# Optimization experiments

Measured on AMD Instinct MI355X. Metric: run time of the kernel, lower is better.

Reference implementation:

```python
import jax, jax.numpy as jnp
import numpy as np

DIM = 1024; DEPTH = 4; HEADS = 16; DIM_HEAD = 64
INNER = HEADS * DIM_HEAD            # 1024
N_LAT = 64; N_MP = 4; MAX_SEQ = 512
FF_MULT = 4; HID = DIM * FF_MULT    # 4096
B = 32; SEQ = 512
EPS = 1e-5


def _custom_ln(x, g):
    # LayerNorm with gain only (module's custom LayerNorm), biased variance
    mean = x.mean(-1, keepdims=True)
    var = x.var(-1, keepdims=True)
    return (x - mean) * jax.lax.rsqrt(var + EPS) * g


def _std_ln(x, w, b):
    # torch nn.LayerNorm with weight and bias
    mean = x.mean(-1, keepdims=True)
    var = x.var(-1, keepdims=True)
    return (x - mean) * jax.lax.rsqrt(var + EPS) * w + b


def setup_inputs() -> dict:
    key = jax.random.key(0)
    ks = jax.random.split(key, 12)
    w = lambda k, shape: jax.random.normal(k, shape, jnp.float32) * 0.02
    return {
        "x": jax.random.normal(ks[0], (B, SEQ, DIM), jnp.float32),
        "mask": jnp.ones((B, SEQ), dtype=bool),
        "pos_emb": w(ks[1], (MAX_SEQ, DIM)),
        "latents": jax.random.normal(ks[2], (N_LAT, DIM), jnp.float32),
        "mp_ln_g": jnp.ones((DIM,), jnp.float32),
        "mp_w": w(ks[3], (DIM, DIM * N_MP)),
        "mp_b": jnp.zeros((DIM * N_MP,), jnp.float32),
        "attn_norm_w": jnp.ones((DEPTH, DIM), jnp.float32),
        "attn_norm_b": jnp.zeros((DEPTH, DIM), jnp.float32),
        "attn_lat_w": jnp.ones((DEPTH, DIM), jnp.float32),
        "attn_lat_b": jnp.zeros((DEPTH, DIM), jnp.float32),
        "Wq": w(ks[4], (DEPTH, DIM, INNER)),
        "Wkv": w(ks[5], (DEPTH, DIM, 2 * INNER)),
        "Wout": w(ks[6], (DEPTH, INNER, DIM)),
        "out_ln_w": jnp.ones((DEPTH, DIM), jnp.float32),
        "out_ln_b": jnp.zeros((DEPTH, DIM), jnp.float32),
        "ff_ln1_g": jnp.ones((DEPTH, DIM), jnp.float32),
        "ff_w1": w(ks[7], (DEPTH, DIM, HID)),
        "ff_ln2_g": jnp.ones((DEPTH, HID), jnp.float32),
        "ff_w2": w(ks[8], (DEPTH, HID, DIM)),
    }


def _forward(x, mask, pos_emb, latents, mp_ln_g, mp_w, mp_b,
             attn_norm_w, attn_norm_b, attn_lat_w, attn_lat_b,
             Wq, Wkv, Wout, out_ln_w, out_ln_b,
             ff_ln1_g, ff_w1, ff_ln2_g, ff_w2):
    b, n, d = x.shape
    x_pos = x + pos_emb[:n]                              # [b, n, d]
    lat = jnp.broadcast_to(latents, (b,) + latents.shape)  # [b, 64, d]

    # latents from mean-pooled sequence (mask in torch code is all-ones)
    pooled = x.mean(axis=1)                              # [b, d]
    mp_lat = (_custom_ln(pooled, mp_ln_g) @ mp_w + mp_b).reshape(b, N_MP, d)
    lat = jnp.concatenate([mp_lat, lat], axis=1)         # [b, 68, d]
    n_lat = lat.shape[1]

    scale = DIM_HEAD ** -0.5
    pad_mask = jnp.pad(mask, ((0, 0), (0, n_lat)), constant_values=True)  # [b, n+68]
    neg = -jnp.finfo(jnp.float32).max

    def split_heads(t):
        return t.reshape(b, -1, HEADS, DIM_HEAD).transpose(0, 2, 1, 3)  # b h n d

    for i in range(DEPTH):
        # --- PerceiverAttention ---
        xn = _std_ln(x_pos, attn_norm_w[i], attn_norm_b[i])
        ln_ = _std_ln(lat, attn_lat_w[i], attn_lat_b[i])
        q = split_heads(ln_ @ Wq[i]) * scale
        kv = jnp.concatenate([xn, ln_], axis=1) @ Wkv[i]   # [b, n+68, 2*inner]
        k, v = jnp.split(kv, 2, axis=-1)
        k = split_heads(k); v = split_heads(v)
        sim = jnp.einsum('bhid,bhjd->bhij', q, k)          # [b, h, 68, n+68]
        sim = jnp.where(pad_mask[:, None, None, :], sim, neg)
        attn = jax.nn.softmax(sim.astype(jnp.float32), axis=-1).astype(sim.dtype)
        out = jnp.einsum('bhij,bhjd->bhid', attn, v)
        out = out.transpose(0, 2, 1, 3).reshape(b, n_lat, INNER)
        lat = _std_ln(out @ Wout[i], out_ln_w[i], out_ln_b[i]) + lat
        # --- FeedForward ---
        h = _custom_ln(lat, ff_ln1_g[i]) @ ff_w1[i]
        h = jax.nn.gelu(h, approximate=False)              # torch nn.GELU default
        h = _custom_ln(h, ff_ln2_g[i]) @ ff_w2[i]
        lat = h + lat
    return lat


def reference(x, mask, pos_emb, latents, mp_ln_g, mp_w, mp_b,
              attn_norm_w, attn_norm_b, attn_lat_w, attn_lat_b,
              Wq, Wkv, Wout, out_ln_w, out_ln_b,
              ff_ln1_g, ff_w1, ff_ln2_g, ff_w2):
    return _forward(x, mask, pos_emb, latents, mp_ln_g, mp_w, mp_b,
                    attn_norm_w, attn_norm_b, attn_lat_w, attn_lat_b,
                    Wq, Wkv, Wout, out_ln_w, out_ln_b,
                    ff_ln1_g, ff_w1, ff_ln2_g, ff_w2)
```

## Files before the change

kernel.cpp:

```cpp
#include <hip/hip_runtime.h>


typedef __attribute__((ext_vector_type(4))) float f32x4;
typedef __attribute__((ext_vector_type(8))) __bf16 bf16x8;
typedef __attribute__((ext_vector_type(4))) __bf16 bf16x4;

#define BATCH 32
#define SEQL  512
#define DIM   1024
#define HEADS 16
#define DH    64
#define LTOT  68
#define KEYS  580
#define KPAD  640
#define HID   4096
#define LN_EPS 1e-5f
#define MLAT  2176

__device__ __forceinline__ float bf2f(__bf16 v) { return (float)v; }
__device__ __forceinline__ __bf16 f2bf(float v) { return (__bf16)v; }
__device__ __forceinline__ float gelu_f(float v) {
    return 0.5f * v * (1.0f + erff(v * 0.70710678118654752f));
}

__device__ __forceinline__ void gld_lds16(const __bf16* g, __bf16* l) {
    __builtin_amdgcn_global_load_lds(
        (const __attribute__((address_space(1))) void*)g,
        (__attribute__((address_space(3))) void*)l, 16, 0, 0);
}

#define SBAR()   asm volatile("s_barrier" ::: "memory")
#define VMCNT4() asm volatile("s_waitcnt vmcnt(4)" ::: "memory")

__device__ __forceinline__ void block_reduce2(float& a, float& b, float* red) {
#pragma unroll
    for (int m = 32; m > 0; m >>= 1) {
        a += __shfl_xor(a, m, 64);
        b += __shfl_xor(b, m, 64);
    }
    int wid = threadIdx.x >> 6, lane = threadIdx.x & 63;
    __syncthreads();
    if (lane == 0) { red[wid] = a; red[4 + wid] = b; }
    __syncthreads();
    a = red[0] + red[1] + red[2] + red[3];
    b = red[4] + red[5] + red[6] + red[7];
}

__global__ __launch_bounds__(256) void add_pos(const float* __restrict__ x,
                                               const float* __restrict__ pos,
                                               __bf16* __restrict__ xp) {
    const int total4 = (BATCH * SEQL * DIM) / 4;
    const int pos4m = (SEQL * DIM) / 4 - 1;
    for (int i = blockIdx.x * 256 + threadIdx.x; i < total4; i += gridDim.x * 256) {
        f32x4 xv = ((const f32x4*)x)[i];
        f32x4 pv = ((const f32x4*)pos)[i & pos4m];
        bf16x4 o;
#pragma unroll
        for (int j = 0; j < 4; ++j) o[j] = f2bf(xv[j] + pv[j]);
        ((bf16x4*)xp)[i] = o;
    }
}

__global__ __launch_bounds__(256) void pool_mean(const float* __restrict__ x,
                                                 float* __restrict__ pooled) {
    int b = blockIdx.x >> 2;
    int d = ((blockIdx.x & 3) << 8) + threadIdx.x;
    const float* p = x + (size_t)b * SEQL * DIM + d;
    float s = 0.f;
    for (int ss = 0; ss < SEQL; ++ss) s += p[(size_t)ss * DIM];
    pooled[b * DIM + d] = s * (1.f / SEQL);
}

__global__ __launch_bounds__(256) void lat_fill(const float* __restrict__ latents,
                                                float* __restrict__ lat) {
    int i = blockIdx.x * 256 + threadIdx.x;
    int b = i >> 14;
    int rem = i & 16383;
    int r = rem >> 8, d4 = rem & 255;
    ((f32x4*)lat)[(size_t)(b * LTOT + 4 + r) * 256 + d4] = ((const f32x4*)latents)[rem];
}

template <typename Tin, bool STD, int COLS>
__global__ __launch_bounds__(256) void ln_rows(const Tin* __restrict__ in,
                                               __bf16* __restrict__ out,
                                               const float* __restrict__ w,
                                               const float* __restrict__ bb) {
    __shared__ float red[8];
    constexpr int NPT = COLS / 256;
    size_t base = (size_t)blockIdx.x * COLS;
    int t = threadIdx.x;
    int c0 = t * NPT;
    float xv[NPT];
    float s = 0.f, s2 = 0.f;
#pragma unroll
    for (int k4 = 0; k4 < NPT / 4; ++k4) {
        if constexpr (sizeof(Tin) == 2) {
            bf16x4 v = *(const bf16x4*)(in + base + c0 + k4 * 4);
#pragma unroll
            for (int e = 0; e < 4; ++e) {
                float f = bf2f(v[e]);
                xv[k4 * 4 + e] = f; s += f; s2 += f * f;
            }
        } else {
            f32x4 v = *(const f32x4*)((const float*)in + base + c0 + k4 * 4);
#pragma unroll
            for (int e = 0; e < 4; ++e) {
                float f = v[e];
                xv[k4 * 4 + e] = f; s += f; s2 += f * f;
            }
        }
    }
    block_reduce2(s, s2, red);
    float mean = s * (1.f / COLS);
    float var = s2 * (1.f / COLS) - mean * mean;
    float rstd = rsqrtf(var + LN_EPS);
#pragma unroll
    for (int k4 = 0; k4 < NPT / 4; ++k4) {
        f32x4 wv = *(const f32x4*)(w + c0 + k4 * 4);
        f32x4 bv;
        if (STD) bv = *(const f32x4*)(bb + c0 + k4 * 4);
        bf16x4 o;
#pragma unroll
        for (int e = 0; e < 4; ++e) {
            float y = (xv[k4 * 4 + e] - mean) * rstd * wv[e];
            if (STD) y += bv[e];
            o[e] = f2bf(y);
        }
        *(bf16x4*)(out + base + c0 + k4 * 4) = o;
    }
}

__global__ __launch_bounds__(256) void ln_gelu2(const __bf16* __restrict__ pk,
                                                __bf16* __restrict__ out,
                                                const float* __restrict__ g) {
    __shared__ float red[8];
    constexpr int NPT = HID / 256;
    const size_t S = (size_t)MLAT * HID;
    size_t base = (size_t)blockIdx.x * HID;
    int t = threadIdx.x;
    int c0 = t * NPT;
    float xv[NPT];
    float s = 0.f, s2 = 0.f;
#pragma unroll
    for (int k4 = 0; k4 < NPT / 4; ++k4) {
        bf16x4 va = *(const bf16x4*)(pk + base + c0 + k4 * 4);
        bf16x4 vb = *(const bf16x4*)(pk + S + base + c0 + k4 * 4);
#pragma unroll
        for (int e = 0; e < 4; ++e) {
            float f = gelu_f(bf2f(va[e]) + bf2f(vb[e]));
            xv[k4 * 4 + e] = f; s += f; s2 += f * f;
        }
    }
    block_reduce2(s, s2, red);
    float mean = s * (1.f / HID);
    float var = s2 * (1.f / HID) - mean * mean;
    float rstd = rsqrtf(var + LN_EPS);
#pragma unroll
    for (int k4 = 0; k4 < NPT / 4; ++k4) {
        f32x4 gv = *(const f32x4*)(g + c0 + k4 * 4);
        bf16x4 o;
#pragma unroll
        for (int e = 0; e < 4; ++e)
            o[e] = f2bf((xv[k4 * 4 + e] - mean) * rstd * gv[e]);
        *(bf16x4*)(out + base + c0 + k4 * 4) = o;
    }
}

__global__ __launch_bounds__(256) void wout_ln_res(const __bf16* __restrict__ gin,
                                                   float* __restrict__ lat,
                                                   __bf16* __restrict__ ffin,
                                                   const float* __restrict__ w,
                                                   const float* __restrict__ b,
                                                   const float* __restrict__ g1) {
    __shared__ float red[8];
    const size_t SL = (size_t)MLAT * DIM;
    size_t base = (size_t)blockIdx.x * DIM;
    int t = threadIdx.x;
    float xv[4];
    float s = 0.f, s2 = 0.f;
#pragma unroll
    for (int k = 0; k < 4; ++k) {
        size_t idx = base + t + (k << 8);
        float v = bf2f(gin[idx]) + bf2f(gin[idx + SL]) +
                  bf2f(gin[idx + 2 * SL]) + bf2f(gin[idx + 3 * SL]);
        xv[k] = v; s += v; s2 += v * v;
    }
    block_reduce2(s, s2, red);
    float mean = s * (1.f / DIM);
    float var = s2 * (1.f / DIM) - mean * mean;
    float rstd = rsqrtf(var + LN_EPS);
    float yv[4];
    s = 0.f; s2 = 0.f;
#pragma unroll
    for (int k = 0; k < 4; ++k) {
        int c = t + (k << 8);
        float y = (xv[k] - mean) * rstd * w[c] + b[c] + lat[base + c];
        yv[k] = y; s += y; s2 += y * y;
        lat[base + c] = y;
    }
    block_reduce2(s, s2, red);
    float mean2 = s * (1.f / DIM);
    float var2 = s2 * (1.f / DIM) - mean2 * mean2;
    float rstd2 = rsqrtf(var2 + LN_EPS);
#pragma unroll
    for (int k = 0; k < 4; ++k) {
        int c = t + (k << 8);
        ffin[base + c] = f2bf((yv[k] - mean2) * rstd2 * g1[c]);
    }
}

__global__ __launch_bounds__(256) void qkv_red(const __bf16* __restrict__ pk,
                                               __bf16* __restrict__ qb,
                                               __bf16* __restrict__ kvb) {
    const size_t S = (size_t)MLAT * 3072;
    int row = blockIdx.y;
    int n = (blockIdx.x * 256 + threadIdx.x) * 4;
    size_t idx = (size_t)row * 3072 + n;
    bf16x4 a = *(const bf16x4*)(pk + idx);
    bf16x4 b = *(const bf16x4*)(pk + S + idx);
    bf16x4 o;
    if (n < 1024) {
#pragma unroll
        for (int e = 0; e < 4; ++e) o[e] = f2bf((bf2f(a[e]) + bf2f(b[e])) * 0.125f);
        *(bf16x4*)(qb + (size_t)row * 1024 + n) = o;
    } else {
#pragma unroll
        for (int e = 0; e < 4; ++e) o[e] = f2bf(bf2f(a[e]) + bf2f(b[e]));
        int bb = ((row >> 2) * 61681) >> 20;
        int r = row - bb * 68;
        *(bf16x4*)(kvb + (size_t)bb * KEYS * 2048 + (size_t)(512 + r) * 2048 +
                   (n - 1024)) = o;
    }
}

__global__ __launch_bounds__(256) void splitk_add8(const __bf16* __restrict__ p,
                                                   float* __restrict__ lat) {
    const size_t S = (size_t)MLAT * 1024;
    int i = blockIdx.x * 256 + threadIdx.x;
    size_t e0 = (size_t)i * 4;
    f32x4 acc = ((f32x4*)lat)[i];
#pragma unroll
    for (int s = 0; s < 8; ++s) {
        bf16x4 v = *(const bf16x4*)(p + s * S + e0);
#pragma unroll
        for (int e = 0; e < 4; ++e) acc[e] += bf2f(v[e]);
    }
    ((f32x4*)lat)[i] = acc;
}

__global__ __launch_bounds__(256) void transpose_all(
    const float* __restrict__ Wq, const float* __restrict__ Wkv,
    const float* __restrict__ Wout, const float* __restrict__ f1,
    const float* __restrict__ f2,
    __bf16* __restrict__ wqT, __bf16* __restrict__ wkvT,
    __bf16* __restrict__ woutT, __bf16* __restrict__ f1T,
    __bf16* __restrict__ f2T) {
    __shared__ float tile[32][33];
    int bid = blockIdx.x;
    const float* in; __bf16* out; int N, nxs, ti;
    if (bid < 1024)      { in = Wq;  out = wqT;  N = 1024; nxs = 5; ti = bid; }
    else if (bid < 3072) { in = Wkv; out = wkvT; N = 2048; nxs = 6; ti = bid - 1024; }
    else if (bid < 4096) { in = Wout;out = woutT;N = 1024; nxs = 5; ti = bid - 3072; }
    else if (bid < 8192) { in = f1;  out = f1T;  N = 4096; nxs = 7; ti = bid - 4096; }
    else                 { in = f2;  out = f2T;  N = 1024; nxs = 5; ti = bid - 8192; }
    int K = (bid >= 8192) ? 4096 : 1024;
    int n0 = (ti & ((1 << nxs) - 1)) << 5;
    int k0 = (ti >> nxs) << 5;
    int tx = threadIdx.x & 31, ty = threadIdx.x >> 5;
#pragma unroll
    for (int p = 0; p < 4; ++p) {
        int kk = ty + p * 8;
        tile[kk][tx] = in[(size_t)(k0 + kk) * N + n0 + tx];
    }
    __syncthreads();
#pragma unroll
    for (int p = 0; p < 4; ++p) {
        int nn = ty + p * 8;
        out[(size_t)(n0 + nn) * K + k0 + tx] = f2bf(tile[tx][nn]);
    }
}

__global__ __launch_bounds__(256) void transpose_cast(const float* __restrict__ in,
                                                      __bf16* __restrict__ out,
                                                      int K, int N) {
    __shared__ float tile[32][33];
    int n0 = blockIdx.x * 32, k0 = blockIdx.y * 32;
    int tx = threadIdx.x & 31, ty = threadIdx.x >> 5;
#pragma unroll
    for (int p = 0; p < 4; ++p) {
        int kk = ty + p * 8;
        tile[kk][tx] = in[(size_t)(k0 + kk) * N + n0 + tx];
    }
    __syncthreads();
#pragma unroll
    for (int p = 0; p < 4; ++p) {
        int nn = ty + p * 8;
        out[(size_t)(n0 + nn) * K + k0 + tx] = f2bf(tile[tx][nn]);
    }
}

template <int EPI, bool POW2>
__global__ __launch_bounds__(256) void gemm_bf16(
    const __bf16* __restrict__ A, const __bf16* __restrict__ Bt,
    void* __restrict__ C0, void* __restrict__ C1, const float* __restrict__ bias,
    int M, int N, int K, int lda, int ldb, int brs, long long bstride, int ldc,
    float scale, int az, long long cz, int zhalf) {
    __shared__ __bf16 As[128][64];
    __shared__ __bf16 Bs[128][64];
    const int t = threadIdx.x;
    const int m0 = blockIdx.y * 128, n0 = blockIdx.x * 128;
    const int z = blockIdx.z;
    A += (size_t)z * az;
    Bt += (size_t)z * az;
    void* Cout = (z < zhalf) ? C0 : C1;
    const long long zoff = (long long)(z < zhalf ? z : z - zhalf) * cz;
    const int wid = t >> 6, lane = t & 63;
    const int wr = wid >> 1, wc = wid & 1;
    const int lrow = lane & 15;
    const int lr = lane >> 3, lc = lane & 7;
    const int src_col = (lc ^ lr) << 3;
    f32x4 acc[4][4] = {};

    int garow[4], gbrow[4];
#pragma unroll
    for (int it = 0; it < 4; ++it) {
        int r = wid * 8 + it * 32 + lr;
        int gm = m0 + r; garow[it] = gm < M ? gm : M - 1;
        int gn = n0 + r; gbrow[it] = gn < N ? gn : N - 1;
    }

    for (int kt = 0; kt < K; kt += 64) {
#pragma unroll
        for (int it = 0; it < 4; ++it) {
            int rb = wid * 8 + it * 32;
            gld_lds16(A + (size_t)garow[it] * lda + kt + src_col, &As[rb][0]);
            gld_lds16(Bt + (size_t)gbrow[it] * ldb + kt + src_col, &Bs[rb][0]);
        }
        __syncthreads();
#pragma unroll
        for (int kc = 0; kc < 2; ++kc) {
            const int ck = (kc << 2) + (lane >> 4);
            bf16x8 af[4], bfr[4];
#pragma unroll
            for (int f = 0; f < 4; ++f) {
                int ra = wr * 64 + f * 16 + lrow;
                af[f] = *(const bf16x8*)(&As[ra][(ck ^ (ra & 7)) << 3]);
                int rb = wc * 64 + f * 16 + lrow;
                bfr[f] = *(const bf16x8*)(&Bs[rb][(ck ^ (rb & 7)) << 3]);
            }
#pragma unroll
            for (int fm = 0; fm < 4; ++fm)
#pragma unroll
                for (int fn = 0; fn < 4; ++fn)
                    acc[fm][fn] = __builtin_amdgcn_mfma_f32_16x16x32_bf16(
                        af[fm], bfr[fn], acc[fm][fn], 0, 0, 0);
        }
        __syncthreads();
    }
    const int rbase = (lane >> 4) << 2;
    const int cofs = lane & 15;
    const int msk = POW2 ? (int)((1u << brs) - 1u) : 0;
#pragma unroll
    for (int fm = 0; fm < 4; ++fm) {
#pragma unroll
        for (int j = 0; j < 4; ++j) {
            int m = m0 + wr * 64 + fm * 16 + rbase + j;
            if (m >= M) continue;
            long long roff;
            if (POW2) roff = (long long)(m >> brs) * bstride + (long long)(m & msk) * ldc;
            else      roff = (long long)(m / brs) * bstride + (long long)(m % brs) * ldc;
            roff += zoff;
#pragma unroll
            for (int fn = 0; fn < 4; ++fn) {
                int n = n0 + wc * 64 + fn * 16 + cofs;
                if (n >= N) continue;
                float v = acc[fm][fn][j];
                if (bias) v += bias[n];
                if (EPI == 0) ((float*)Cout)[roff + n] = v;
                else if (EPI == 1) ((__bf16*)Cout)[roff + n] = f2bf(v);
                else if (EPI == 2) ((__bf16*)Cout)[roff + n] = f2bf(v * scale);
                else ((float*)Cout)[roff + n] = gelu_f(v);
            }
        }
    }
}

template <int EPI>
__global__ __launch_bounds__(512, 2) void gemm256(
    const __bf16* __restrict__ A, const __bf16* __restrict__ Bt,
    void* __restrict__ Cout, const float* __restrict__ bias,
    int M, int N, int K, int brs, long long bstride, int ldc, float scale,
    int gxs) {
    __shared__ __bf16 As[2][256][64];
    __shared__ __bf16 Bs[2][256][64];
    const int t = threadIdx.x;
    const int wid = t >> 6, lane = t & 63;
    const int wr = wid >> 2, wc = wid & 3;
    const int lrow = lane & 15, lk = lane >> 4;
    const int lr8 = lane >> 3;
    const int scol = ((lane & 7) ^ lr8) << 3;

    int nwg = gridDim.x;
    int L = blockIdx.x;
    if ((nwg & 7) == 0) L = (L & 7) * (nwg >> 3) + (L >> 3);
    const int bx = L & ((1 << gxs) - 1), by = L >> gxs;
    const int m0 = by * 256, n0 = bx * 256;

    unsigned aoff[4], boff[4];
#pragma unroll
    for (int h = 0; h < 2; ++h)
#pragma unroll
        for (int rnd = 0; rnd < 2; ++rnd) {
            int r = h * 128 + rnd * 64 + wid * 8 + lr8;
            int gm = m0 + r; if (gm > M - 1) gm = M - 1;
            aoff[h * 2 + rnd] = (unsigned)(gm * K + scol);
            int gn = n0 + r; if (gn > N - 1) gn = N - 1;
            boff[h * 2 + rnd] = (unsigned)(gn * K + scol);
        }

    auto stgA = [&](int buf, int tile, int h) {
        int kt = tile << 6;
        gld_lds16(A + aoff[h * 2 + 0] + kt, &As[buf][h * 128 + wid * 8][0]);
        gld_lds16(A + aoff[h * 2 + 1] + kt, &As[buf][h * 128 + 64 + wid * 8][0]);
    };
    auto stgB = [&](int buf, int tile, int h) {
        int kt = tile << 6;
        gld_lds16(Bt + boff[h * 2 + 0] + kt, &Bs[buf][h * 128 + wid * 8][0]);
        gld_lds16(Bt + boff[h * 2 + 1] + kt, &Bs[buf][h * 128 + 64 + wid * 8][0]);
    };

    f32x4 acc[8][4] = {};
    bf16x8 AF0[4][2], AF1[4][2], BF[2][2], BF2[2][2];

    auto rdAF = [&](bf16x8 (&AF)[4][2], int buf, int qm) {
#pragma unroll
        for (int i = 0; i < 4; ++i) {
            int ra = wr * 128 + (qm * 4 + i) * 16 + lrow;
            AF[i][0] = *(const bf16x8*)(&As[buf][ra][((lk) ^ (ra & 7)) << 3]);
            AF[i][1] = *(const bf16x8*)(&As[buf][ra][((4 + lk) ^ (ra & 7)) << 3]);
        }
    };
    auto rdBF = [&](bf16x8 (&BV)[2][2], int buf, int qn) {
#pragma unroll
        for (int i = 0; i < 2; ++i) {
            int rb = wc * 64 + (qn * 2 + i) * 16 + lrow;
            BV[i][0] = *(const bf16x8*)(&Bs[buf][rb][((lk) ^ (rb & 7)) << 3]);
            BV[i][1] = *(const bf16x8*)(&Bs[buf][rb][((4 + lk) ^ (rb & 7)) << 3]);
        }
    };
    auto mfq = [&](bf16x8 (&AF)[4][2], bf16x8 (&BV)[2][2], int mo, int no) {
        __builtin_amdgcn_s_setprio(1);
#pragma unroll
        for (int i = 0; i < 4; ++i)
#pragma unroll
            for (int nf = 0; nf < 2; ++nf)
#pragma unroll
                for (int ks = 0; ks < 2; ++ks)
                    acc[mo + i][no + nf] = __builtin_amdgcn_mfma_f32_16x16x32_bf16(
                        AF[i][ks], BV[nf][ks], acc[mo + i][no + nf], 0, 0, 0);
        __builtin_amdgcn_s_setprio(0);
    };

    const int nt = K >> 6;
    stgA(0, 0, 0); stgA(0, 0, 1);
    stgB(0, 0, 0); stgB(0, 0, 1);
    stgA(1, 1, 0); stgA(1, 1, 1);
    VMCNT4();
    SBAR();

    for (int tt = 0; tt < nt; tt += 2) {
        const int t1 = tt + 1;
        const int t2 = (tt + 2 < nt) ? tt + 2 : nt - 1;
        const int t3 = (tt + 3 < nt) ? tt + 3 : nt - 1;
        rdAF(AF0, 0, 0); rdBF(BF, 0, 0);
        stgB(1, t1, 0);
        SBAR();
        mfq(AF0, BF, 0, 0);
        SBAR();
        rdAF(AF1, 0, 1);
        stgB(1, t1, 1);
        SBAR();
        mfq(AF1, BF, 4, 0);
        SBAR();
        rdBF(BF2, 0, 1);
        stgA(0, t2, 0);
        SBAR();
        mfq(AF1, BF2, 4, 2);
        SBAR();
        stgA(0, t2, 1);
        SBAR();
        mfq(AF0, BF2, 0, 2);
        VMCNT4();
        SBAR();
        rdAF(AF0, 1, 0); rdBF(BF, 1, 0);
        stgB(0, t2, 0);
        SBAR();
        mfq(AF0, BF, 0, 0);
        SBAR();
        rdAF(AF1, 1, 1);
        stgB(0, t2, 1);
        SBAR();
        mfq(AF1, BF, 4, 0);
        SBAR();
        rdBF(BF2, 1, 1);
        stgA(1, t3, 0);
        SBAR();
        mfq(AF1, BF2, 4, 2);
        SBAR();
        stgA(1, t3, 1);
        SBAR();
        mfq(AF0, BF2, 0, 2);
        VMCNT4();
        SBAR();
    }

    const int rbase = (lane >> 4) << 2;
    const int cofs = lane & 15;
    const int msk = (int)((1u << brs) - 1u);
#pragma unroll
    for (int mf = 0; mf < 8; ++mf) {
#pragma unroll
        for (int j = 0; j < 4; ++j) {
            int m = m0 + wr * 128 + mf * 16 + rbase + j;
            if (m >= M) continue;
            long long roff = (long long)(m >> brs) * bstride +
                             (long long)(m & msk) * ldc;
#pragma unroll
            for (int nf = 0; nf < 4; ++nf) {
                int n = n0 + wc * 64 + nf * 16 + cofs;
                if (n >= N) continue;
                float v = acc[mf][nf][j];
                if (bias) v += bias[n];
                if (EPI == 1) ((__bf16*)Cout)[roff + n] = f2bf(v);
                else if (EPI == 3) ((float*)Cout)[roff + n] = gelu_f(v);
                else ((float*)Cout)[roff + n] = v;
            }
        }
    }
}

__global__ __launch_bounds__(256) void vt_tr(const __bf16* __restrict__ kv,
                                             __bf16* __restrict__ vt) {
    __shared__ __bf16 tile[32][34];
    const int bh = blockIdx.x, b = bh >> 4, h = bh & 15;
    const int k0 = blockIdx.y * 32, d0 = blockIdx.z * 32;
    const int tx = threadIdx.x & 31, ty = threadIdx.x >> 5;
    const __bf16* vbase = kv + (size_t)b * KEYS * 2048 + 1024 + h * DH;
#pragma unroll
    for (int p = 0; p < 4; ++p) {
        int kk = k0 + ty + p * 8;
        int kc = kk < KEYS ? kk : KEYS - 1;
        tile[ty + p * 8][tx] = vbase[(size_t)kc * 2048 + d0 + tx];
    }
    __syncthreads();
    __bf16* obase = vt + (size_t)bh * DH * KPAD;
#pragma unroll
    for (int p = 0; p < 4; ++p) {
        int nn = ty + p * 8;
        __bf16 val = (k0 + tx < KEYS) ? tile[tx][nn] : (__bf16)0.f;
        obase[(size_t)(d0 + nn) * KPAD + k0 + tx] = val;
    }
}

__global__ __launch_bounds__(256) void fused_attn(const __bf16* __restrict__ q,
                                                  const __bf16* __restrict__ kv,
                                                  const __bf16* __restrict__ vt,
                                                  __bf16* __restrict__ ao) {
    __shared__ __bf16 Qs[80][64];
    __shared__ __bf16 Ks[2][64][64];
    __shared__ __bf16 Ps[80][640];
    __shared__ float rowpm[4][80];
    __shared__ float rowm[80];
    __shared__ float rowl[80];

    const int bh = blockIdx.x, b = bh >> 4, h = bh & 15;
    const int t = threadIdx.x, w = t >> 6, lane = t & 63;
    const int lrow = lane & 15;
    const int rbase = (lane >> 4) << 2, cofs = lane & 15;
    const int lr = lane >> 3, lc = lane & 7;
    const int src_col = (lc ^ lr) << 3;

    const __bf16* qbase = q + (size_t)b * LTOT * DIM + h * DH;
    const bf16x8 zero8 = {};
    for (int s = t; s < 80 * 8; s += 256) {
        int r = s >> 3, c8 = s & 7;
        bf16x8 v = zero8;
        if (r < LTOT) v = *(const bf16x8*)(qbase + (size_t)r * DIM + (c8 << 3));
        *(bf16x8*)(&Qs[r][(c8 ^ (r & 7)) << 3]) = v;
    }

    const __bf16* kbase = kv + (size_t)b * KEYS * 2048 + h * DH;
    const __bf16* vbase = vt + (size_t)bh * DH * KPAD;

    auto stageK = [&](int buf, int kt) {
#pragma unroll
        for (int rnd = 0; rnd < 2; ++rnd) {
            int r8 = w * 16 + rnd * 8;
            int gk = kt * 64 + r8 + lr; if (gk > KEYS - 1) gk = KEYS - 1;
            gld_lds16(kbase + (size_t)gk * 2048 + src_col, &Ks[buf][r8][0]);
        }
    };
    auto stageV = [&](int buf, int kt) {
#pragma unroll
        for (int rnd = 0; rnd < 2; ++rnd) {
            int r8 = w * 16 + rnd * 8;
            gld_lds16(vbase + (size_t)(r8 + lr) * KPAD + kt * 64 + src_col,
                      &Ks[buf][r8][0]);
        }
    };

    float pmax[5][4];
#pragma unroll
    for (int fm = 0; fm < 5; ++fm)
#pragma unroll
        for (int j = 0; j < 4; ++j) pmax[fm][j] = -3.0e38f;

    stageK(0, 0);
    __syncthreads();
    for (int kt = 0; kt < 10; ++kt) {
        if (kt < 9) stageK((kt + 1) & 1, kt + 1);
        f32x4 acc[5] = {};
#pragma unroll
        for (int kc = 0; kc < 2; ++kc) {
            int ck = (kc << 2) + (lane >> 4);
            int rb = w * 16 + lrow;
            bf16x8 bfr = *(const bf16x8*)(&Ks[kt & 1][rb][(ck ^ (rb & 7)) << 3]);
#pragma unroll
            for (int fm = 0; fm < 5; ++fm) {
                int ra = fm * 16 + lrow;
                bf16x8 af = *(const bf16x8*)(&Qs[ra][(ck ^ (ra & 7)) << 3]);
                acc[fm] = __builtin_amdgcn_mfma_f32_16x16x32_bf16(
                    af, bfr, acc[fm], 0, 0, 0);
            }
        }
        int key = kt * 64 + w * 16 + cofs;
        int c8 = key >> 3, e = key & 7;
#pragma unroll
        for (int fm = 0; fm < 5; ++fm) {
#pragma unroll
            for (int j = 0; j < 4; ++j) {
                int qrow = fm * 16 + rbase + j;
                float v = (key < KEYS) ? acc[fm][j] : -1.0e30f;
                pmax[fm][j] = fmaxf(pmax[fm][j], v);
                int swz = ((c8 & 7) ^ (qrow & 7)) | (c8 & ~7);
                Ps[qrow][swz * 8 + e] = f2bf(v);
            }
        }
        __syncthreads();
    }
#pragma unroll
    for (int fm = 0; fm < 5; ++fm)
#pragma unroll
        for (int j = 0; j < 4; ++j) {
            float m = pmax[fm][j];
            m = fmaxf(m, __shfl_xor(m, 1, 64));
            m = fmaxf(m, __shfl_xor(m, 2, 64));
            m = fmaxf(m, __shfl_xor(m, 4, 64));
            m = fmaxf(m, __shfl_xor(m, 8, 64));
            if (cofs == 0) rowpm[w][fm * 16 + rbase + j] = m;
        }
    __syncthreads();
    if (t < 80)
        rowm[t] = fmaxf(fmaxf(rowpm[0][t], rowpm[1][t]),
                        fmaxf(rowpm[2][t], rowpm[3][t]));
    __syncthreads();

    for (int rr = t >> 2; rr < LTOT; rr += 64) {
        int c4 = t & 3;
        float m = rowm[rr];
        float lsum = 0.f;
#pragma unroll
        for (int cc = 0; cc < 20; ++cc) {
            int c8 = c4 * 20 + cc;
            int swz = ((c8 & 7) ^ (rr & 7)) | (c8 & ~7);
            bf16x8 v = *(bf16x8*)(&Ps[rr][swz * 8]);
            bf16x8 o;
#pragma unroll
            for (int e = 0; e < 8; ++e) {
                float p = __expf(bf2f(v[e]) - m);
                lsum += p;
                o[e] = f2bf(p);
            }
            *(bf16x8*)(&Ps[rr][swz * 8]) = o;
        }
        lsum += __shfl_xor(lsum, 1, 64);
        lsum += __shfl_xor(lsum, 2, 64);
        if (c4 == 0) rowl[rr] = lsum;
    }

    stageV(0, 0);
    __syncthreads();
    f32x4 oacc[5] = {};
    for (int kt = 0; kt < 10; ++kt) {
        if (kt < 9) stageV((kt + 1) & 1, kt + 1);
#pragma unroll
        for (int kc = 0; kc < 2; ++kc) {
            int ck = (kc << 2) + (lane >> 4);
            int rb = w * 16 + lrow;
            bf16x8 bfr = *(const bf16x8*)(&Ks[kt & 1][rb][(ck ^ (rb & 7)) << 3]);
            int gc8 = kt * 8 + ck;
#pragma unroll
            for (int fm = 0; fm < 5; ++fm) {
                int ra = fm * 16 + lrow;
                int swz = ((gc8 & 7) ^ (ra & 7)) | (gc8 & ~7);
                bf16x8 af = *(const bf16x8*)(&Ps[ra][swz * 8]);
                oacc[fm] = __builtin_amdgcn_mfma_f32_16x16x32_bf16(
                    af, bfr, oacc[fm], 0, 0, 0);
            }
        }
        __syncthreads();
    }
    __bf16* obase = ao + (size_t)b * LTOT * DIM + h * DH;
#pragma unroll
    for (int fm = 0; fm < 5; ++fm)
#pragma unroll
        for (int j = 0; j < 4; ++j) {
            int qrow = fm * 16 + rbase + j;
            if (qrow >= LTOT) continue;
            float inv = 1.f / rowl[qrow];
            obase[(size_t)qrow * DIM + w * 16 + cofs] = f2bf(oacc[fm][j] * inv);
        }
}

template <int EPI, bool POW2>
static void g128(const __bf16* A, const __bf16* Bt, void* C0, void* C1,
                 const float* bias, int M, int N, int K, int lda, int ldb,
                 int brs, long long bs, int ldc, float scale, int gz, int az,
                 long long cz, int zhalf, hipStream_t s) {
    dim3 g(N / 128, (M + 127) / 128, gz);
    gemm_bf16<EPI, POW2><<<g, 256, 0, s>>>(A, Bt, C0, C1, bias, M, N, K, lda,
                                           ldb, brs, bs, ldc, scale, az, cz,
                                           zhalf);
}

extern "C" void kernel_launch(void* const* d_in, const int* in_sizes, int n_in,
                              void* d_out, int out_size, void* d_ws, size_t ws_size,
                              hipStream_t stream) {
    (void)in_sizes; (void)n_in; (void)out_size; (void)ws_size;
    const float* x          = (const float*)d_in[0];
    const float* pos_emb    = (const float*)d_in[2];
    const float* latents    = (const float*)d_in[3];
    const float* mp_ln_g    = (const float*)d_in[4];
    const float* mp_w       = (const float*)d_in[5];
    const float* mp_b       = (const float*)d_in[6];
    const float* attn_norm_w= (const float*)d_in[7];
    const float* attn_norm_b= (const float*)d_in[8];
    const float* attn_lat_w = (const float*)d_in[9];
    const float* attn_lat_b = (const float*)d_in[10];
    const float* Wq         = (const float*)d_in[11];
    const float* Wkv        = (const float*)d_in[12];
    const float* Wout       = (const float*)d_in[13];
    const float* out_ln_w   = (const float*)d_in[14];
    const float* out_ln_b   = (const float*)d_in[15];
    const float* ff_ln1_g   = (const float*)d_in[16];
    const float* ff_w1      = (const float*)d_in[17];
    const float* ff_ln2_g   = (const float*)d_in[18];
    const float* ff_w2      = (const float*)d_in[19];

    float* lat = (float*)d_out;

    char* ws = (char*)d_ws;
    size_t off = 0;
    auto take = [&](size_t bytes) -> char* {
        char* p = ws + off;
        off += (bytes + 255) & ~(size_t)255;
        return p;
    };
    __bf16* xpos = (__bf16*)take(2ULL * BATCH * SEQL * DIM);
    __bf16* xn   = (__bf16*)take(2ULL * BATCH * SEQL * DIM);
    __bf16* lnl  = (__bf16*)take(2ULL * BATCH * LTOT * DIM);
    __bf16* ffin = (__bf16*)take(2ULL * BATCH * LTOT * DIM);
    __bf16* qb   = (__bf16*)take(2ULL * BATCH * LTOT * DIM);
    __bf16* ao   = (__bf16*)take(2ULL * BATCH * LTOT * DIM);
    __bf16* kvb  = (__bf16*)take(2ULL * BATCH * KEYS * 2048);
    float*  gout = (float*)take(4ULL * MLAT * HID);
    __bf16* h2   = (__bf16*)take(2ULL * MLAT * HID);
    __bf16* vt   = (__bf16*)take(2ULL * BATCH * HEADS * DH * KPAD);
    __bf16* wT   = (__bf16*)take(2ULL * 12 * 1024 * 1024);
    float*  pooled = (float*)take(4ULL * BATCH * DIM);
    __bf16* mpin = (__bf16*)take(2ULL * BATCH * DIM);

    __bf16* gkb = (__bf16*)gout;

    __bf16* wqT   = wT;
    __bf16* wkvT  = wT + 1 * 1024 * 1024;
    __bf16* woutT = wT + 3 * 1024 * 1024;
    __bf16* f1T   = wT + 4 * 1024 * 1024;
    __bf16* f2T   = wT + 8 * 1024 * 1024;
    __bf16* mpwT  = wT;

    add_pos<<<4096, 256, 0, stream>>>(x, pos_emb, xpos);
    pool_mean<<<128, 256, 0, stream>>>(x, pooled);
    ln_rows<float, false, DIM><<<BATCH, 256, 0, stream>>>(pooled, mpin, mp_ln_g, nullptr);
    transpose_cast<<<dim3(128, 32), 256, 0, stream>>>(mp_w, mpwT, 1024, 4096);
    g128<0, true>(mpin, mpwT, lat, lat, mp_b, BATCH, 4096, 1024, 1024, 1024,
                  5, 0, LTOT * DIM, 1.f, 1, 0, 0, 1, stream);
    lat_fill<<<2048, 256, 0, stream>>>(latents, lat);

    for (int i = 0; i < 4; ++i) {
        transpose_all<<<12288, 256, 0, stream>>>(
            Wq + (size_t)i * 1024 * 1024, Wkv + (size_t)i * 1024 * 2048,
            Wout + (size_t)i * 1024 * 1024, ff_w1 + (size_t)i * 1024 * 4096,
            ff_w2 + (size_t)i * 4096 * 1024,
            wqT, wkvT, woutT, f1T, f2T);

        ln_rows<__bf16, true, DIM><<<BATCH * SEQL, 256, 0, stream>>>(
            xpos, xn, attn_norm_w + i * DIM, attn_norm_b + i * DIM);
        ln_rows<float, true, DIM><<<BATCH * LTOT, 256, 0, stream>>>(
            lat, lnl, attn_lat_w + i * DIM, attn_lat_b + i * DIM);

        g128<1, true>(lnl, wqT, gkb, gkb, nullptr, MLAT, 3072, 512, 1024, 1024,
                      31, 0, 3072, 1.f, 2, 512, (long long)MLAT * 3072, 2, stream);
        qkv_red<<<dim3(3, MLAT), 256, 0, stream>>>(gkb, qb, kvb);

        gemm256<1><<<dim3(512), 512, 0, stream>>>(
            xn, wkvT, kvb, nullptr, BATCH * SEQL, 2048, 1024,
            9, (long long)KEYS * 2048, 2048, 1.f, 3);

        vt_tr<<<dim3(BATCH * HEADS, KPAD / 32, 2), 256, 0, stream>>>(kvb, vt);
        fused_attn<<<BATCH * HEADS, 256, 0, stream>>>(qb, kvb, vt, ao);

        g128<1, true>(ao, woutT, vt, vt, nullptr, MLAT, 1024, 256, 1024, 1024,
                      31, 0, 1024, 1.f, 4, 256, (long long)MLAT * 1024, 4, stream);
        wout_ln_res<<<BATCH * LTOT, 256, 0, stream>>>(
            vt, lat, ffin, out_ln_w + i * DIM, out_ln_b + i * DIM, ff_ln1_g + i * DIM);

        g128<1, true>(ffin, f1T, gkb, gkb, nullptr, MLAT, HID, 512, 1024, 1024,
                      31, 0, HID, 1.f, 2, 512, (long long)MLAT * HID, 2, stream);
        ln_gelu2<<<BATCH * LTOT, 256, 0, stream>>>(gkb, h2, ff_ln2_g + i * HID);

        g128<1, true>(h2, f2T, gkb, gkb, nullptr, MLAT, 1024, 512, HID, HID,
                      31, 0, 1024, 1.f, 8, 512, (long long)MLAT * 1024, 8, stream);
        splitk_add8<<<MLAT, 256, 0, stream>>>(gkb, lat);
    }
}
```

Baseline: 1.678 ms.

## Hoist layer-invariant input normalization and fold LN affine into KV weights

The context LayerNorm of x+pos is the same for every layer apart from its affine weight and bias. The change computes the normalized x-hat once, instead of re-running ln_rows over the full 16K-row sequence in every layer. Per-layer gamma is folded into a scaled copy of the KV weight matrix during the existing transpose. Beta is folded into a precomputed bias vector (beta·Wkv) that the KV GEMM epilogue adds. Pooling is also split into partial sums fused with the mp LayerNorm; this adds extra weight-copy writes and an atomic-based bias kernel, and changes bf16 rounding order.

```diff
diff --git a/kernel.cpp b/kernel.cpp
--- a/kernel.cpp
+++ b/kernel.cpp
@@ -46,29 +46,71 @@
     b = red[4] + red[5] + red[6] + red[7];
 }
 
-__global__ __launch_bounds__(256) void add_pos(const float* __restrict__ x,
+__global__ __launch_bounds__(256) void nhat_ln(const float* __restrict__ x,
                                                const float* __restrict__ pos,
-                                               __bf16* __restrict__ xp) {
-    const int total4 = (BATCH * SEQL * DIM) / 4;
-    const int pos4m = (SEQL * DIM) / 4 - 1;
-    for (int i = blockIdx.x * 256 + threadIdx.x; i < total4; i += gridDim.x * 256) {
-        f32x4 xv = ((const f32x4*)x)[i];
-        f32x4 pv = ((const f32x4*)pos)[i & pos4m];
-        bf16x4 o;
-#pragma unroll
-        for (int j = 0; j < 4; ++j) o[j] = f2bf(xv[j] + pv[j]);
-        ((bf16x4*)xp)[i] = o;
-    }
-}
-
-__global__ __launch_bounds__(256) void pool_mean(const float* __restrict__ x,
-                                                 float* __restrict__ pooled) {
-    int b = blockIdx.x >> 2;
-    int d = ((blockIdx.x & 3) << 8) + threadIdx.x;
-    const float* p = x + (size_t)b * SEQL * DIM + d;
+                                               __bf16* __restrict__ nh) {
+    __shared__ float red[8];
+    int row = blockIdx.x;
+    int s = row & 511;
+    size_t base = (size_t)row * DIM;
+    const float* prow = pos + (size_t)s * DIM;
+    int t = threadIdx.x;
+    int c0 = t * 4;
+    f32x4 xv = *(const f32x4*)(x + base + c0);
+    f32x4 pv = *(const f32x4*)(prow + c0);
+    float v[4];
+    float sm = 0.f, s2 = 0.f;
+#pragma unroll
+    for (int e = 0; e < 4; ++e) {
+        float f = xv[e] + pv[e];
+        v[e] = f; sm += f; s2 += f * f;
+    }
+    block_reduce2(sm, s2, red);
+    float mean = sm * (1.f / DIM);
+    float var = s2 * (1.f / DIM) - mean * mean;
+    float rstd = rsqrtf(var + LN_EPS);
+    bf16x4 o;
+#pragma unroll
+    for (int e = 0; e < 4; ++e) o[e] = f2bf((v[e] - mean) * rstd);
+    *(bf16x4*)(nh + base + c0) = o;
+}
+
+__global__ __launch_bounds__(256) void pool_part(const float* __restrict__ x,
+                                                 float* __restrict__ part) {
+    int b = blockIdx.x >> 2, dc = blockIdx.x & 3;
+    int sc = blockIdx.y;
+    int d = dc * 256 + threadIdx.x;
+    const float* p = x + (size_t)b * SEQL * DIM + (size_t)sc * 128 * DIM + d;
     float s = 0.f;
-    for (int ss = 0; ss < SEQL; ++ss) s += p[(size_t)ss * DIM];
-    pooled[b * DIM + d] = s * (1.f / SEQL);
+    for (int ss = 0; ss < 128; ++ss) s += p[(size_t)ss * DIM];
+    part[(size_t)sc * BATCH * DIM + b * DIM + d] = s;
+}
+
+__global__ __launch_bounds__(256) void mp_ln(const float* __restrict__ part,
+                                             __bf16* __restrict__ mpin,
+                                             const float* __restrict__ g) {
+    __shared__ float red[8];
+    int b = blockIdx.x;
+    int t = threadIdx.x;
+    int c0 = t * 4;
+    const size_t S = (size_t)BATCH * DIM;
+    float v[4];
+    float sm = 0.f, s2 = 0.f;
+#pragma unroll
+    for (int e = 0; e < 4; ++e) {
+        int c = c0 + e;
+        float f = (part[b * DIM + c] + part[S + b * DIM + c] +
+                   part[2 * S + b * DIM + c] + part[3 * S + b * DIM + c]) *
+                  (1.f / SEQL);
+        v[e] = f; sm += f; s2 += f * f;
+    }
+    block_reduce2(sm, s2, red);
+    float mean = sm * (1.f / DIM);
+    float var = s2 * (1.f / DIM) - mean * mean;
+    float rstd = rsqrtf(var + LN_EPS);
+#pragma unroll
+    for (int e = 0; e < 4; ++e)
+        mpin[b * DIM + c0 + e] = f2bf((v[e] - mean) * rstd * g[c0 + e]);
 }
 
 __global__ __launch_bounds__(256) void lat_fill(const float* __restrict__ latents,
@@ -78,6 +120,20 @@
     int rem = i & 16383;
     int r = rem >> 8, d4 = rem & 255;
     ((f32x4*)lat)[(size_t)(b * LTOT + 4 + r) * 256 + d4] = ((const f32x4*)latents)[rem];
+}
+
+__global__ __launch_bounds__(256) void kv_bias4(const float* __restrict__ Wkv,
+                                                const float* __restrict__ nb,
+                                                float* __restrict__ out) {
+    int n = blockIdx.x * 256 + threadIdx.x;
+    int k0 = blockIdx.y * 128;
+    int i = blockIdx.z;
+    const float* wb = Wkv + (size_t)i * 1024 * 2048;
+    const float* bb = nb + i * DIM + k0;
+    float s = 0.f;
+    for (int k = 0; k < 128; ++k)
+        s += bb[k] * wb[(size_t)(k0 + k) * 2048 + n];
+    atomicAdd(out + i * 2048 + n, s);
 }
 
 template <typename Tin, bool STD, int COLS>
@@ -251,15 +307,16 @@
 __global__ __launch_bounds__(256) void transpose_all(
     const float* __restrict__ Wq, const float* __restrict__ Wkv,
     const float* __restrict__ Wout, const float* __restrict__ f1,
-    const float* __restrict__ f2,
+    const float* __restrict__ f2, const float* __restrict__ kvw,
     __bf16* __restrict__ wqT, __bf16* __restrict__ wkvT,
     __bf16* __restrict__ woutT, __bf16* __restrict__ f1T,
-    __bf16* __restrict__ f2T) {
+    __bf16* __restrict__ f2T, __bf16* __restrict__ wkvF) {
     __shared__ float tile[32][33];
     int bid = blockIdx.x;
     const float* in; __bf16* out; int N, nxs, ti;
+    bool kv = false;
     if (bid < 1024)      { in = Wq;  out = wqT;  N = 1024; nxs = 5; ti = bid; }
-    else if (bid < 3072) { in = Wkv; out = wkvT; N = 2048; nxs = 6; ti = bid - 1024; }
+    else if (bid < 3072) { in = Wkv; out = wkvT; N = 2048; nxs = 6; ti = bid - 1024; kv = true; }
     else if (bid < 4096) { in = Wout;out = woutT;N = 1024; nxs = 5; ti = bid - 3072; }
     else if (bid < 8192) { in = f1;  out = f1T;  N = 4096; nxs = 7; ti = bid - 4096; }
     else                 { in = f2;  out = f2T;  N = 1024; nxs = 5; ti = bid - 8192; }
@@ -273,10 +330,13 @@
         tile[kk][tx] = in[(size_t)(k0 + kk) * N + n0 + tx];
     }
     __syncthreads();
+    float wk = kv ? kvw[k0 + tx] : 0.f;
 #pragma unroll
     for (int p = 0; p < 4; ++p) {
         int nn = ty + p * 8;
-        out[(size_t)(n0 + nn) * K + k0 + tx] = f2bf(tile[tx][nn]);
+        float v = tile[tx][nn];
+        out[(size_t)(n0 + nn) * K + k0 + tx] = f2bf(v);
+        if (kv) wkvF[(size_t)(n0 + nn) * K + k0 + tx] = f2bf(v * wk);
     }
 }
 
@@ -766,8 +826,7 @@
         off += (bytes + 255) & ~(size_t)255;
         return p;
     };
-    __bf16* xpos = (__bf16*)take(2ULL * BATCH * SEQL * DIM);
-    __bf16* xn   = (__bf16*)take(2ULL * BATCH * SEQL * DIM);
+    __bf16* nhat = (__bf16*)take(2ULL * BATCH * SEQL * DIM);
     __bf16* lnl  = (__bf16*)take(2ULL * BATCH * LTOT * DIM);
     __bf16* ffin = (__bf16*)take(2ULL * BATCH * LTOT * DIM);
     __bf16* qb   = (__bf16*)take(2ULL * BATCH * LTOT * DIM);
@@ -776,8 +835,9 @@
     float*  gout = (float*)take(4ULL * MLAT * HID);
     __bf16* h2   = (__bf16*)take(2ULL * MLAT * HID);
     __bf16* vt   = (__bf16*)take(2ULL * BATCH * HEADS * DH * KPAD);
-    __bf16* wT   = (__bf16*)take(2ULL * 12 * 1024 * 1024);
-    float*  pooled = (float*)take(4ULL * BATCH * DIM);
+    __bf16* wT   = (__bf16*)take(2ULL * 14 * 1024 * 1024);
+    float*  part = (float*)take(4ULL * 4 * BATCH * DIM);
+    float*  kvbias4 = (float*)take(4ULL * 4 * 2048);
     __bf16* mpin = (__bf16*)take(2ULL * BATCH * DIM);
 
     __bf16* gkb = (__bf16*)gout;
@@ -787,11 +847,14 @@
     __bf16* woutT = wT + 3 * 1024 * 1024;
     __bf16* f1T   = wT + 4 * 1024 * 1024;
     __bf16* f2T   = wT + 8 * 1024 * 1024;
+    __bf16* wkvF  = wT + 12 * 1024 * 1024;
     __bf16* mpwT  = wT;
 
-    add_pos<<<4096, 256, 0, stream>>>(x, pos_emb, xpos);
-    pool_mean<<<128, 256, 0, stream>>>(x, pooled);
-    ln_rows<float, false, DIM><<<BATCH, 256, 0, stream>>>(pooled, mpin, mp_ln_g, nullptr);
+    nhat_ln<<<BATCH * SEQL, 256, 0, stream>>>(x, pos_emb, nhat);
+    pool_part<<<dim3(128, 4), 256, 0, stream>>>(x, part);
+    mp_ln<<<BATCH, 256, 0, stream>>>(part, mpin, mp_ln_g);
+    (void)hipMemsetAsync(kvbias4, 0, 4ULL * 4 * 2048, stream);
+    kv_bias4<<<dim3(8, 8, 4), 256, 0, stream>>>(Wkv, attn_norm_b, kvbias4);
     transpose_cast<<<dim3(128, 32), 256, 0, stream>>>(mp_w, mpwT, 1024, 4096);
     g128<0, true>(mpin, mpwT, lat, lat, mp_b, BATCH, 4096, 1024, 1024, 1024,
                   5, 0, LTOT * DIM, 1.f, 1, 0, 0, 1, stream);
@@ -801,11 +864,9 @@
         transpose_all<<<12288, 256, 0, stream>>>(
             Wq + (size_t)i * 1024 * 1024, Wkv + (size_t)i * 1024 * 2048,
             Wout + (size_t)i * 1024 * 1024, ff_w1 + (size_t)i * 1024 * 4096,
-            ff_w2 + (size_t)i * 4096 * 1024,
-            wqT, wkvT, woutT, f1T, f2T);
-
-        ln_rows<__bf16, true, DIM><<<BATCH * SEQL, 256, 0, stream>>>(
-            xpos, xn, attn_norm_w + i * DIM, attn_norm_b + i * DIM);
+            ff_w2 + (size_t)i * 4096 * 1024, attn_norm_w + i * DIM,
+            wqT, wkvT, woutT, f1T, f2T, wkvF);
+
         ln_rows<float, true, DIM><<<BATCH * LTOT, 256, 0, stream>>>(
             lat, lnl, attn_lat_w + i * DIM, attn_lat_b + i * DIM);
 
@@ -814,7 +875,7 @@
         qkv_red<<<dim3(3, MLAT), 256, 0, stream>>>(gkb, qb, kvb);
 
         gemm256<1><<<dim3(512), 512, 0, stream>>>(
-            xn, wkvT, kvb, nullptr, BATCH * SEQL, 2048, 1024,
+            nhat, wkvF, kvb, kvbias4 + i * 2048, BATCH * SEQL, 2048, 1024,
             9, (long long)KEYS * 2048, 2048, 1.f, 3);
 
         vt_tr<<<dim3(BATCH * HEADS, KPAD / 32, 2), 256, 0, stream>>>(kvb, vt);
```

After: 1.703 ms. Within noise of the previous version (+1.5%).

## Convert attention kernel to single-pass online softmax with per-tile rescaling

Applied to the files above, without the earlier changes.

Replaces the two-pass attention (store all scores in a large LDS buffer, then softmax, then a separate PV pass) with a flash-style online softmax. Each key tile computes QK^T, updates the running row max and sum, rescales the output accumulator, and immediately multiplies by a V tile staged in its own double buffer. This cuts LDS use from an 80x640 score buffer to 80x64, which may raise occupancy, and fuses the two key loops. In exchange it adds extra cross-wave reductions and several block barriers per tile.

```diff
diff --git a/kernel.cpp b/kernel.cpp
--- a/kernel.cpp
+++ b/kernel.cpp
@@ -568,15 +568,16 @@
                                                   __bf16* __restrict__ ao) {
     __shared__ __bf16 Qs[80][64];
     __shared__ __bf16 Ks[2][64][64];
-    __shared__ __bf16 Ps[80][640];
+    __shared__ __bf16 Vs[2][64][64];
+    __shared__ __bf16 Ps[80][64];
     __shared__ float rowpm[4][80];
-    __shared__ float rowm[80];
-    __shared__ float rowl[80];
+    __shared__ float rowps[4][80];
+    __shared__ float rowm[80], rowl[80], scl[80];
 
     const int bh = blockIdx.x, b = bh >> 4, h = bh & 15;
     const int t = threadIdx.x, w = t >> 6, lane = t & 63;
-    const int lrow = lane & 15;
-    const int rbase = (lane >> 4) << 2, cofs = lane & 15;
+    const int lrow = lane & 15, lk = lane >> 4;
+    const int rbase = lk << 2, cofs = lane & 15;
     const int lr = lane >> 3, lc = lane & 7;
     const int src_col = (lc ^ lr) << 3;
 
@@ -588,6 +589,7 @@
         if (r < LTOT) v = *(const bf16x8*)(qbase + (size_t)r * DIM + (c8 << 3));
         *(bf16x8*)(&Qs[r][(c8 ^ (r & 7)) << 3]) = v;
     }
+    if (t < 80) { rowm[t] = -3.0e38f; rowl[t] = 0.f; }
 
     const __bf16* kbase = kv + (size_t)b * KEYS * 2048 + h * DH;
     const __bf16* vbase = vt + (size_t)bh * DH * KPAD;
@@ -605,26 +607,24 @@
         for (int rnd = 0; rnd < 2; ++rnd) {
             int r8 = w * 16 + rnd * 8;
             gld_lds16(vbase + (size_t)(r8 + lr) * KPAD + kt * 64 + src_col,
-                      &Ks[buf][r8][0]);
+                      &Vs[buf][r8][0]);
         }
     };
 
-    float pmax[5][4];
-#pragma unroll
-    for (int fm = 0; fm < 5; ++fm)
-#pragma unroll
-        for (int j = 0; j < 4; ++j) pmax[fm][j] = -3.0e38f;
-
+    f32x4 oacc[5] = {};
     stageK(0, 0);
     __syncthreads();
+
     for (int kt = 0; kt < 10; ++kt) {
-        if (kt < 9) stageK((kt + 1) & 1, kt + 1);
+        const int cur = kt & 1;
+        stageV(cur, kt);
+        if (kt < 9) stageK(cur ^ 1, kt + 1);
         f32x4 acc[5] = {};
 #pragma unroll
         for (int kc = 0; kc < 2; ++kc) {
-            int ck = (kc << 2) + (lane >> 4);
+            int ck = (kc << 2) + lk;
             int rb = w * 16 + lrow;
-            bf16x8 bfr = *(const bf16x8*)(&Ks[kt & 1][rb][(ck ^ (rb & 7)) << 3]);
+            bf16x8 bfr = *(const bf16x8*)(&Ks[cur][rb][(ck ^ (rb & 7)) << 3]);
 #pragma unroll
             for (int fm = 0; fm < 5; ++fm) {
                 int ra = fm * 16 + lrow;
@@ -633,77 +633,58 @@
                     af, bfr, acc[fm], 0, 0, 0);
             }
         }
-        int key = kt * 64 + w * 16 + cofs;
-        int c8 = key >> 3, e = key & 7;
-#pragma unroll
-        for (int fm = 0; fm < 5; ++fm) {
+        const int key = kt * 64 + w * 16 + cofs;
+        const bool kvalid = key < KEYS;
+#pragma unroll
+        for (int fm = 0; fm < 5; ++fm)
+#pragma unroll
+            for (int j = 0; j < 4; ++j) {
+                float v = kvalid ? acc[fm][j] : -3.0e38f;
+                v = fmaxf(v, __shfl_xor(v, 1, 64));
+                v = fmaxf(v, __shfl_xor(v, 2, 64));
+                v = fmaxf(v, __shfl_xor(v, 4, 64));
+                v = fmaxf(v, __shfl_xor(v, 8, 64));
+                if (cofs == 0) rowpm[w][fm * 16 + rbase + j] = v;
+            }
+        __syncthreads();
+        if (t < 80) {
+            float tm = fmaxf(fmaxf(rowpm[0][t], rowpm[1][t]),
+                             fmaxf(rowpm[2][t], rowpm[3][t]));
+            float mold = rowm[t];
+            float mnew = fmaxf(mold, tm);
+            rowm[t] = mnew;
+            scl[t] = __expf(mold - mnew);
+        }
+        __syncthreads();
+        const int kloc = w * 16 + cofs;
+        const int c8t = kloc >> 3, e8 = kloc & 7;
+#pragma unroll
+        for (int fm = 0; fm < 5; ++fm)
 #pragma unroll
             for (int j = 0; j < 4; ++j) {
                 int qrow = fm * 16 + rbase + j;
-                float v = (key < KEYS) ? acc[fm][j] : -1.0e30f;
-                pmax[fm][j] = fmaxf(pmax[fm][j], v);
-                int swz = ((c8 & 7) ^ (qrow & 7)) | (c8 & ~7);
-                Ps[qrow][swz * 8 + e] = f2bf(v);
+                float p = kvalid ? __expf(acc[fm][j] - rowm[qrow]) : 0.f;
+                Ps[qrow][(c8t ^ (qrow & 7)) * 8 + e8] = f2bf(p);
+                p += __shfl_xor(p, 1, 64);
+                p += __shfl_xor(p, 2, 64);
+                p += __shfl_xor(p, 4, 64);
+                p += __shfl_xor(p, 8, 64);
+                if (cofs == 0) rowps[w][qrow] = p;
+                oacc[fm][j] *= scl[qrow];
             }
-        }
         __syncthreads();
-    }
-#pragma unroll
-    for (int fm = 0; fm < 5; ++fm)
-#pragma unroll
-        for (int j = 0; j < 4; ++j) {
-            float m = pmax[fm][j];
-            m = fmaxf(m, __shfl_xor(m, 1, 64));
-            m = fmaxf(m, __shfl_xor(m, 2, 64));
-            m = fmaxf(m, __shfl_xor(m, 4, 64));
-            m = fmaxf(m, __shfl_xor(m, 8, 64));
-            if (cofs == 0) rowpm[w][fm * 16 + rbase + j] = m;
-        }
-    __syncthreads();
-    if (t < 80)
-        rowm[t] = fmaxf(fmaxf(rowpm[0][t], rowpm[1][t]),
-                        fmaxf(rowpm[2][t], rowpm[3][t]));
-    __syncthreads();
-
-    for (int rr = t >> 2; rr < LTOT; rr += 64) {
-        int c4 = t & 3;
-        float m = rowm[rr];
-        float lsum = 0.f;
-#pragma unroll
-        for (int cc = 0; cc < 20; ++cc) {
-            int c8 = c4 * 20 + cc;
-            int swz = ((c8 & 7) ^ (rr & 7)) | (c8 & ~7);
-            bf16x8 v = *(bf16x8*)(&Ps[rr][swz * 8]);
-            bf16x8 o;
-#pragma unroll
-            for (int e = 0; e < 8; ++e) {
-                float p = __expf(bf2f(v[e]) - m);
-                lsum += p;
-                o[e] = f2bf(p);
-            }
-            *(bf16x8*)(&Ps[rr][swz * 8]) = o;
-        }
-        lsum += __shfl_xor(lsum, 1, 64);
-        lsum += __shfl_xor(lsum, 2, 64);
-        if (c4 == 0) rowl[rr] = lsum;
-    }
-
-    stageV(0, 0);
-    __syncthreads();
-    f32x4 oacc[5] = {};
-    for (int kt = 0; kt < 10; ++kt) {
-        if (kt < 9) stageV((kt + 1) & 1, kt + 1);
+        if (t < 80)
+            rowl[t] = rowl[t] * scl[t] +
+                      rowps[0][t] + rowps[1][t] + rowps[2][t] + rowps[3][t];
 #pragma unroll
         for (int kc = 0; kc < 2; ++kc) {
-            int ck = (kc << 2) + (lane >> 4);
+            int ck = (kc << 2) + lk;
             int rb = w * 16 + lrow;
-            bf16x8 bfr = *(const bf16x8*)(&Ks[kt & 1][rb][(ck ^ (rb & 7)) << 3]);
-            int gc8 = kt * 8 + ck;
+            bf16x8 bfr = *(const bf16x8*)(&Vs[cur][rb][(ck ^ (rb & 7)) << 3]);
 #pragma unroll
             for (int fm = 0; fm < 5; ++fm) {
                 int ra = fm * 16 + lrow;
-                int swz = ((gc8 & 7) ^ (ra & 7)) | (gc8 & ~7);
-                bf16x8 af = *(const bf16x8*)(&Ps[ra][swz * 8]);
+                bf16x8 af = *(const bf16x8*)(&Ps[ra][(ck ^ (ra & 7)) << 3]);
                 oacc[fm] = __builtin_amdgcn_mfma_f32_16x16x32_bf16(
                     af, bfr, oacc[fm], 0, 0, 0);
             }
```

New measurement: 1.749 ms. +4.2%, slower.
